# Kernel optimization log

Hardware: AMD Instinct MI355X
Metric: run time of the kernel (lower is better)

## Reference

```python
import jax, jax.numpy as jnp
import numpy as np

D_IN, D_HID, D_OUT, ITERS = 768, 256, 64, 5
LN_EPS = 1e-5


def setup_inputs() -> dict:
    key = jax.random.key(0)
    ks = jax.random.split(key, 8)
    B = 131072
    s = lambda n: 1.0 / np.sqrt(n)
    return {
        "z_mantis": jax.random.normal(ks[0], (B, D_IN), dtype=jnp.float32),
        "W1": jax.random.normal(ks[1], (D_HID, D_IN), dtype=jnp.float32) * s(D_IN),
        "b1": jnp.zeros((D_HID,), jnp.float32),
        "ln_g": jnp.ones((D_HID,), jnp.float32),
        "ln_b": jnp.zeros((D_HID,), jnp.float32),
        "W2": jax.random.normal(ks[2], (D_OUT, D_HID), dtype=jnp.float32) * s(D_HID),
        "b2": jnp.zeros((D_OUT,), jnp.float32),
        "Wr": jax.random.normal(ks[3], (D_OUT, D_IN), dtype=jnp.float32) * s(D_IN),
        "br": jnp.zeros((D_OUT,), jnp.float32),
        "Wo": jnp.linalg.qr(jax.random.normal(ks[4], (D_OUT, D_OUT), dtype=jnp.float32))[0],
        "Wv": jax.random.normal(ks[5], (D_OUT, D_OUT), dtype=jnp.float32) * s(D_OUT),
        "bv": jnp.zeros((D_OUT,), jnp.float32),
        "Wm": jax.random.normal(ks[6], (D_OUT, D_OUT), dtype=jnp.float32) * s(D_OUT),
        "bm": jnp.full((D_OUT,), 3.0, jnp.float32),
        "scale": jnp.full((1,), 2.0, jnp.float32),
    }


def _newton_schulz_whitening(X):
    # X: [B, D], returns whitened X and whitening matrix W (both [.., D])
    B, D = X.shape
    mu = jnp.mean(X, axis=0, keepdims=True)
    Xc = X - mu
    denom = jnp.float32(B - 1 if B > 1 else 1)
    sigma = (Xc.T @ Xc) / denom + 0.001 * jnp.eye(D, dtype=X.dtype)
    sigma_norm = jnp.trace(sigma) * 1.5 + 1e-6
    sigma_scaled = sigma / sigma_norm
    I = jnp.eye(D, dtype=X.dtype)
    W = I
    for _ in range(ITERS):
        P = W @ sigma_scaled @ W.T
        W = (1.5 * I - 0.5 * P) @ W
    X_white = (Xc / jnp.sqrt(sigma_norm)) @ W.T
    return X_white, W


def reference(z_mantis, W1, b1, ln_g, ln_b, W2, b2, Wr, br, Wo, Wv, bv, Wm, bm, scale):
    # pre_mlp: Linear -> LayerNorm -> GELU -> (Dropout=id in eval) -> Linear
    h = z_mantis @ W1.T + b1
    mean = jnp.mean(h, axis=-1, keepdims=True)
    var = jnp.var(h, axis=-1, keepdims=True)
    h = (h - mean) / jnp.sqrt(var + LN_EPS) * ln_g + ln_b
    h = jax.nn.gelu(h, approximate=False)
    h_latent = h @ W2.T + b2
    h_latent = h_latent + (z_mantis @ Wr.T + br)  # residual projection
    h_orth = h_latent @ Wo.T
    # B = 131072 > D_OUT, so whitening branch is always taken
    h_white, _ = _newton_schulz_whitening(h_orth)
    val = h_white @ Wv.T + bv
    mask = jax.nn.sigmoid(h_white @ Wm.T + bm)
    return val * mask * scale
```

## Files before the change

### kernel.cpp

```cpp
#include <hip/hip_runtime.h>
#include <hip/hip_bf16.h>
#include <math.h>


typedef __attribute__((ext_vector_type(8))) short short8;
typedef __attribute__((ext_vector_type(4))) float f32x4;

#define NB 131072
#define DIN 768
#define DHID 256
#define DOUT 64
#define LN_EPS 1e-5f

__device__ __forceinline__ unsigned short f2bf(float f) {
    union { float f; unsigned u; } v; v.f = f;
    return (unsigned short)((v.u + 0x7FFFu + ((v.u >> 16) & 1u)) >> 16);
}
__device__ __forceinline__ unsigned short f2bf_hu(float f) {
    return (unsigned short)((__float_as_uint(f) + 0x8000u) >> 16);
}
__device__ __forceinline__ unsigned pk2bf(float a, float b) {
    unsigned ua = __float_as_uint(a) + 0x8000u;
    unsigned ub = __float_as_uint(b) + 0x8000u;
    return __builtin_amdgcn_perm(ub, ua, 0x07060302u);
}

__global__ void k_cvt_w1(const float* __restrict__ W1, unsigned short* __restrict__ W1bf) {
    int i = blockIdx.x * 256 + threadIdx.x;
    float4 v = reinterpret_cast<const float4*>(W1)[i];
    ushort4 o;
    o.x = f2bf(v.x); o.y = f2bf(v.y); o.z = f2bf(v.z); o.w = f2bf(v.w);
    reinterpret_cast<ushort4*>(W1bf)[i] = o;
}

__global__ void k_fuse_w(const float* __restrict__ Wo, const float* __restrict__ W2,
                         const float* __restrict__ Wr, const float* __restrict__ b2,
                         const float* __restrict__ br,
                         unsigned short* __restrict__ Wabf, unsigned short* __restrict__ Wbbf,
                         float* __restrict__ c0) {
    int idx = blockIdx.x * 256 + threadIdx.x;
    if (idx < DOUT * DIN) {
        int i = idx / DIN, k = idx % DIN;
        float s = 0.f;
        #pragma unroll 8
        for (int j = 0; j < 64; j++) s += Wo[i * 64 + j] * Wr[j * DIN + k];
        Wbbf[idx] = f2bf(s);
    } else if (idx < DOUT * DIN + DOUT * DHID) {
        int e = idx - DOUT * DIN;
        int i = e / DHID, k = e % DHID;
        float s = 0.f;
        #pragma unroll 8
        for (int j = 0; j < 64; j++) s += Wo[i * 64 + j] * W2[j * DHID + k];
        Wabf[e] = f2bf(s);
    } else if (idx < DOUT * DIN + DOUT * DHID + DOUT) {
        int i = idx - (DOUT * DIN + DOUT * DHID);
        float s = 0.f;
        for (int j = 0; j < 64; j++) s += Wo[i * 64 + j] * (b2[j] + br[j]);
        c0[i] = s;
    }
}

#define ZSTR_U 20
#define ZBUF_U (64 * ZSTR_U)
#define HP_STR 264
__launch_bounds__(256, 2)
__global__ void k_main(const float* __restrict__ z,
                       const unsigned short* __restrict__ W1bf,
                       const unsigned short* __restrict__ Wbbf,
                       const unsigned short* __restrict__ Wabf,
                       const float* __restrict__ c0,
                       const float* __restrict__ b1,
                       const float* __restrict__ ln_g,
                       const float* __restrict__ ln_b,
                       float* __restrict__ X) {
    __shared__ __align__(16) unsigned smem_u[2 * ZBUF_U + (64 * HP_STR) / 2 + 256 + 256 + 64 + 64];
    unsigned* zbf = smem_u;
    unsigned short* hp = (unsigned short*)(smem_u + 2 * ZBUF_U);
    float* red1  = (float*)(smem_u + 2 * ZBUF_U + (64 * HP_STR) / 2);
    float* red2  = red1 + 256;
    float* meanb = red2 + 256;
    float* rstdb = meanb + 64;

    const int tid  = threadIdx.x;
    const int w    = tid >> 6;
    const int lane = tid & 63;
    const int q    = lane >> 4;
    const int l15  = lane & 15;
    const int m0   = blockIdx.x * 64;

    const int sr = tid >> 2;
    const int sc = (tid & 3) * 8;
    const float* zrow = z + (size_t)(m0 + sr) * DIN + sc;
    const unsigned widx = sr * ZSTR_U + (tid & 3) * 4;

    f32x4 acc1[4][4];
    f32x4 accR[4];
    #pragma unroll
    for (int mt = 0; mt < 4; mt++) {
        accR[mt] = (f32x4){0.f, 0.f, 0.f, 0.f};
        #pragma unroll
        for (int nt = 0; nt < 4; nt++) acc1[mt][nt] = (f32x4){0.f, 0.f, 0.f, 0.f};
    }

    {
        float4 f0 = *reinterpret_cast<const float4*>(zrow);
        float4 f1 = *reinterpret_cast<const float4*>(zrow + 4);
        uint4 pk = { pk2bf(f0.x, f0.y), pk2bf(f0.z, f0.w), pk2bf(f1.x, f1.y), pk2bf(f1.z, f1.w) };
        *reinterpret_cast<uint4*>(&zbf[widx]) = pk;
    }
    short8 wc[5];
    #pragma unroll
    for (int nt = 0; nt < 4; nt++)
        wc[nt] = *reinterpret_cast<const short8*>(W1bf + (size_t)(64 * w + 16 * nt + l15) * DIN + q * 8);
    wc[4] = *reinterpret_cast<const short8*>(Wbbf + (size_t)(16 * w + l15) * DIN + q * 8);
    __syncthreads();

    for (int k0 = 0; k0 < 24; k0++) {
        const int buf = k0 & 1;
        float4 g0 = {0, 0, 0, 0}, g1 = {0, 0, 0, 0};
        short8 wn[5];
        if (k0 < 23) {
            const float* zp = zrow + (k0 + 1) * 32;
            g0 = *reinterpret_cast<const float4*>(zp);
            g1 = *reinterpret_cast<const float4*>(zp + 4);
            const int kn = (k0 + 1) * 32 + q * 8;
            #pragma unroll
            for (int nt = 0; nt < 4; nt++)
                wn[nt] = *reinterpret_cast<const short8*>(W1bf + (size_t)(64 * w + 16 * nt + l15) * DIN + kn);
            wn[4] = *reinterpret_cast<const short8*>(Wbbf + (size_t)(16 * w + l15) * DIN + kn);
        }
        short8 a[4];
        #pragma unroll
        for (int mt = 0; mt < 4; mt++)
            a[mt] = *reinterpret_cast<const short8*>(&zbf[buf * ZBUF_U + (16 * mt + l15) * ZSTR_U + q * 4]);
        #pragma unroll
        for (int mt = 0; mt < 4; mt++) {
            accR[mt] = __builtin_amdgcn_mfma_f32_16x16x32_bf16(a[mt], wc[4], accR[mt], 0, 0, 0);
            #pragma unroll
            for (int nt = 0; nt < 4; nt++)
                acc1[mt][nt] = __builtin_amdgcn_mfma_f32_16x16x32_bf16(a[mt], wc[nt], acc1[mt][nt], 0, 0, 0);
        }
        if (k0 < 23) {
            uint4 pk = { pk2bf(g0.x, g0.y), pk2bf(g0.z, g0.w), pk2bf(g1.x, g1.y), pk2bf(g1.z, g1.w) };
            *reinterpret_cast<uint4*>(&zbf[(buf ^ 1) * ZBUF_U + widx]) = pk;
            #pragma unroll
            for (int i = 0; i < 5; i++) wc[i] = wn[i];
        }
        __syncthreads();
    }

    float b1v[4], gv[4], betav[4];
    #pragma unroll
    for (int nt = 0; nt < 4; nt++) {
        int col = 64 * w + 16 * nt + l15;
        b1v[nt] = b1[col]; gv[nt] = ln_g[col]; betav[nt] = ln_b[col];
    }
    #pragma unroll
    for (int mt = 0; mt < 4; mt++) {
        #pragma unroll
        for (int r = 0; r < 4; r++) {
            float s1 = 0.f, s2 = 0.f;
            #pragma unroll
            for (int nt = 0; nt < 4; nt++) {
                float x = acc1[mt][nt][r] + b1v[nt];
                s1 += x; s2 += x * x;
            }
            #pragma unroll
            for (int off = 1; off < 16; off <<= 1) {
                s1 += __shfl_xor(s1, off, 64);
                s2 += __shfl_xor(s2, off, 64);
            }
            if (l15 == 0) {
                int row = 16 * mt + 4 * q + r;
                red1[w * 64 + row] = s1; red2[w * 64 + row] = s2;
            }
        }
    }
    __syncthreads();
    if (tid < 64) {
        float s1 = red1[tid] + red1[64 + tid] + red1[128 + tid] + red1[192 + tid];
        float s2 = red2[tid] + red2[64 + tid] + red2[128 + tid] + red2[192 + tid];
        float mean = s1 * (1.f / 256.f);
        float var  = s2 * (1.f / 256.f) - mean * mean;
        meanb[tid] = mean;
        rstdb[tid] = rsqrtf(var + LN_EPS);
    }
    __syncthreads();

    #pragma unroll
    for (int mt = 0; mt < 4; mt++) {
        #pragma unroll
        for (int r = 0; r < 4; r++) {
            int row = 16 * mt + 4 * q + r;
            float mean = meanb[row], rstd = rstdb[row];
            #pragma unroll
            for (int nt = 0; nt < 4; nt++) {
                float x = acc1[mt][nt][r] + b1v[nt];
                float y = (x - mean) * rstd * gv[nt] + betav[nt];
                float g = 0.5f * y * (1.0f + erff(y * 0.70710678118654752f));
                hp[row * HP_STR + 64 * w + 16 * nt + l15] = f2bf_hu(g);
            }
        }
    }
    short8 wa_c = *reinterpret_cast<const short8*>(Wabf + (size_t)(16 * w + l15) * DHID + q * 8);
    __syncthreads();

    f32x4 acc2[4];
    #pragma unroll
    for (int mt = 0; mt < 4; mt++) acc2[mt] = accR[mt];
    for (int k = 0; k < 8; k++) {
        short8 wa_n;
        if (k < 7)
            wa_n = *reinterpret_cast<const short8*>(Wabf + (size_t)(16 * w + l15) * DHID + (k + 1) * 32 + q * 8);
        #pragma unroll
        for (int mt = 0; mt < 4; mt++) {
            short8 af = *reinterpret_cast<const short8*>(&hp[(16 * mt + l15) * HP_STR + k * 32 + q * 8]);
            acc2[mt] = __builtin_amdgcn_mfma_f32_16x16x32_bf16(af, wa_c, acc2[mt], 0, 0, 0);
        }
        if (k < 7) wa_c = wa_n;
    }
    float c0v = c0[16 * w + l15];
    #pragma unroll
    for (int mt = 0; mt < 4; mt++) {
        #pragma unroll
        for (int r = 0; r < 4; r++)
            X[(size_t)(m0 + 16 * mt + 4 * q + r) * 64 + 16 * w + l15] = acc2[mt][r] + c0v;
    }
}

__global__ void k_stats(const float* __restrict__ X, float* __restrict__ colsum,
                        float* __restrict__ XtX) {
    __shared__ float Xs[64 * 64];
    __shared__ float csb[256];
    const int t = threadIdx.x;
    const int ti = t >> 4, tj = t & 15;
    float acc[4][4] = {{0.f}};
    float cs = 0.f;
    const int base = blockIdx.x * 512;
    for (int c = 0; c < 8; c++) {
        __syncthreads();
        #pragma unroll
        for (int kk = 0; kk < 4; kk++) {
            int fi = t + 256 * kk;
            reinterpret_cast<float4*>(Xs)[fi] =
                reinterpret_cast<const float4*>(X + (size_t)(base + c * 64) * 64)[fi];
        }
        __syncthreads();
        #pragma unroll 2
        for (int r = 0; r < 64; r++) {
            float4 xa = *reinterpret_cast<const float4*>(&Xs[r * 64 + 4 * ti]);
            float4 xb = *reinterpret_cast<const float4*>(&Xs[r * 64 + 4 * tj]);
            acc[0][0] += xa.x * xb.x; acc[0][1] += xa.x * xb.y; acc[0][2] += xa.x * xb.z; acc[0][3] += xa.x * xb.w;
            acc[1][0] += xa.y * xb.x; acc[1][1] += xa.y * xb.y; acc[1][2] += xa.y * xb.z; acc[1][3] += xa.y * xb.w;
            acc[2][0] += xa.z * xb.x; acc[2][1] += xa.z * xb.y; acc[2][2] += xa.z * xb.z; acc[2][3] += xa.z * xb.w;
            acc[3][0] += xa.w * xb.x; acc[3][1] += xa.w * xb.y; acc[3][2] += xa.w * xb.z; acc[3][3] += xa.w * xb.w;
        }
        {
            int col = t & 63, r0 = (t >> 6) * 16;
            float s = 0.f;
            #pragma unroll
            for (int r = r0; r < r0 + 16; r++) s += Xs[r * 64 + col];
            cs += s;
        }
    }
    #pragma unroll
    for (int a = 0; a < 4; a++)
        #pragma unroll
        for (int b = 0; b < 4; b++)
            atomicAdd(&XtX[(4 * ti + a) * 64 + 4 * tj + b], acc[a][b]);
    csb[t] = cs;
    __syncthreads();
    if (t < 64) atomicAdd(&colsum[t], csb[t] + csb[t + 64] + csb[t + 128] + csb[t + 192]);
}

#define NSTR 68
__device__ __forceinline__ void mm64(float* __restrict__ C, const float* __restrict__ A,
                                     const float* __restrict__ B, int ti, int tj) {
    float acc[4][4] = {{0.f}};
    #pragma unroll 2
    for (int k = 0; k < 64; k += 4) {
        float4 av[4], bv[4];
        #pragma unroll
        for (int p = 0; p < 4; p++) av[p] = *reinterpret_cast<const float4*>(&A[(4 * ti + p) * NSTR + k]);
        #pragma unroll
        for (int kk = 0; kk < 4; kk++) bv[kk] = *reinterpret_cast<const float4*>(&B[(k + kk) * NSTR + 4 * tj]);
        #pragma unroll
        for (int p = 0; p < 4; p++) {
            acc[p][0] += av[p].x * bv[0].x + av[p].y * bv[1].x + av[p].z * bv[2].x + av[p].w * bv[3].x;
            acc[p][1] += av[p].x * bv[0].y + av[p].y * bv[1].y + av[p].z * bv[2].y + av[p].w * bv[3].y;
            acc[p][2] += av[p].x * bv[0].z + av[p].y * bv[1].z + av[p].z * bv[2].z + av[p].w * bv[3].z;
            acc[p][3] += av[p].x * bv[0].w + av[p].y * bv[1].w + av[p].z * bv[2].w + av[p].w * bv[3].w;
        }
    }
    #pragma unroll
    for (int p = 0; p < 4; p++)
        #pragma unroll
        for (int r = 0; r < 4; r++) C[(4 * ti + p) * NSTR + 4 * tj + r] = acc[p][r];
    __syncthreads();
}

__global__ void k_ns(const float* __restrict__ XtX, const float* __restrict__ colsum,
                     const float* __restrict__ Wv, const float* __restrict__ bv,
                     const float* __restrict__ Wm, const float* __restrict__ bm,
                     unsigned short* __restrict__ AvTbf, unsigned short* __restrict__ AmTbf,
                     float* __restrict__ cv, float* __restrict__ cm) {
    __shared__ __align__(16) float Mb[64 * NSTR], Gb[64 * NSTR], G2b[64 * NSTR],
                                   Fb[64 * NSTR], Tb[64 * NSTR];
    __shared__ float mu[64];
    __shared__ float snorm;
    const int t = threadIdx.x;
    const int ti = t >> 4, tj = t & 15;

    if (t < 64) mu[t] = colsum[t] * (1.f / (float)NB);
    __syncthreads();
    for (int idx = t; idx < 4096; idx += 256) {
        int i = idx >> 6, j = idx & 63;
        float s = (XtX[idx] - (float)NB * mu[i] * mu[j]) * (1.f / (float)(NB - 1));
        if (i == j) s += 0.001f;
        Mb[i * NSTR + j] = s;
    }
    __syncthreads();
    if (t == 0) {
        float tr = 0.f;
        for (int i = 0; i < 64; i++) tr += Mb[i * NSTR + i];
        snorm = tr * 1.5f + 1e-6f;
    }
    __syncthreads();
    const float sn = snorm;
    for (int idx = t; idx < 4096; idx += 256) {
        int i = idx >> 6, j = idx & 63;
        Mb[i * NSTR + j] /= sn;
    }
    __syncthreads();

    float *M = Mb, *G = Gb, *G2 = G2b, *F = Fb, *T = Tb;
    for (int it = 0; it < 5; it++) {
        for (int idx = t; idx < 4096; idx += 256) {
            int i = idx >> 6, j = idx & 63;
            G[i * NSTR + j] = (i == j ? 1.5f : 0.f) - 0.5f * M[i * NSTR + j];
        }
        __syncthreads();
        if (it == 0) {
            for (int idx = t; idx < 4096; idx += 256) {
                int i = idx >> 6, j = idx & 63;
                F[i * NSTR + j] = G[i * NSTR + j];
            }
            __syncthreads();
        } else {
            mm64(T, F, G, ti, tj);
            float* tmp = F; F = T; T = tmp;
        }
        if (it < 4) {
            mm64(G2, G, G, ti, tj);
            mm64(T, M, G2, ti, tj);
            float* tmp = M; M = T; T = tmp;
        }
    }
    const float rsn = rsqrtf(sn);
    float accv[4][4] = {{0.f}}, accm[4][4] = {{0.f}};
    #pragma unroll 2
    for (int k = 0; k < 64; k += 4) {
        float4 av[4];
        #pragma unroll
        for (int p = 0; p < 4; p++) av[p] = *reinterpret_cast<const float4*>(&F[(4 * ti + p) * NSTR + k]);
        #pragma unroll
        for (int r = 0; r < 4; r++) {
            float4 wv4 = *reinterpret_cast<const float4*>(&Wv[(size_t)(4 * tj + r) * 64 + k]);
            float4 wm4 = *reinterpret_cast<const float4*>(&Wm[(size_t)(4 * tj + r) * 64 + k]);
            #pragma unroll
            for (int p = 0; p < 4; p++) {
                accv[p][r] += av[p].x * wv4.x + av[p].y * wv4.y + av[p].z * wv4.z + av[p].w * wv4.w;
                accm[p][r] += av[p].x * wm4.x + av[p].y * wm4.y + av[p].z * wm4.z + av[p].w * wm4.w;
            }
        }
    }
    #pragma unroll
    for (int p = 0; p < 4; p++)
        #pragma unroll
        for (int r = 0; r < 4; r++) {
            AvTbf[(4 * tj + r) * 64 + 4 * ti + p] = f2bf_hu(rsn * accv[p][r]);
            AmTbf[(4 * tj + r) * 64 + 4 * ti + p] = f2bf_hu(rsn * accm[p][r]);
        }
    #pragma unroll
    for (int r = 0; r < 4; r++) {
        float pv = 0.f, pm = 0.f;
        #pragma unroll
        for (int p = 0; p < 4; p++) {
            pv += mu[4 * ti + p] * accv[p][r];
            pm += mu[4 * ti + p] * accm[p][r];
        }
        G2b[ti * 64 + 4 * tj + r] = pv * rsn;
        Gb[ti * 64 + 4 * tj + r]  = pm * rsn;
    }
    __syncthreads();
    if (t < 64) {
        float a = bv[t], b = bm[t];
        for (int i = 0; i < 16; i++) {
            a -= G2b[i * 64 + t];
            b -= Gb[i * 64 + t];
        }
        cv[t] = a; cm[t] = b;
    }
}

__global__ void k_out(const float* __restrict__ X,
                      const unsigned short* __restrict__ AvTbf,
                      const unsigned short* __restrict__ AmTbf,
                      const float* __restrict__ cv, const float* __restrict__ cm,
                      const float* __restrict__ scale, float* __restrict__ out) {
    const int tid  = threadIdx.x;
    const int w    = tid >> 6;
    const int lane = tid & 63;
    const int q    = lane >> 4;
    const int l15  = lane & 15;
    const int base = blockIdx.x * 64 + w * 16;

    short8 bfv[4][2], bfm[4][2];
    #pragma unroll
    for (int nt = 0; nt < 4; nt++)
        #pragma unroll
        for (int kk = 0; kk < 2; kk++) {
            bfv[nt][kk] = *reinterpret_cast<const short8*>(AvTbf + (16 * nt + l15) * 64 + kk * 32 + q * 8);
            bfm[nt][kk] = *reinterpret_cast<const short8*>(AmTbf + (16 * nt + l15) * 64 + kk * 32 + q * 8);
        }
    f32x4 av_[4], am_[4];
    #pragma unroll
    for (int nt = 0; nt < 4; nt++) {
        av_[nt] = (f32x4){0.f, 0.f, 0.f, 0.f};
        am_[nt] = (f32x4){0.f, 0.f, 0.f, 0.f};
    }
    #pragma unroll
    for (int kk = 0; kk < 2; kk++) {
        const float* xp = X + (size_t)(base + l15) * 64 + kk * 32 + q * 8;
        float4 f0 = *reinterpret_cast<const float4*>(xp);
        float4 f1 = *reinterpret_cast<const float4*>(xp + 4);
        union { unsigned u[4]; short8 s; } pk;
        pk.u[0] = pk2bf(f0.x, f0.y); pk.u[1] = pk2bf(f0.z, f0.w);
        pk.u[2] = pk2bf(f1.x, f1.y); pk.u[3] = pk2bf(f1.z, f1.w);
        #pragma unroll
        for (int nt = 0; nt < 4; nt++) {
            av_[nt] = __builtin_amdgcn_mfma_f32_16x16x32_bf16(pk.s, bfv[nt][kk], av_[nt], 0, 0, 0);
            am_[nt] = __builtin_amdgcn_mfma_f32_16x16x32_bf16(pk.s, bfm[nt][kk], am_[nt], 0, 0, 0);
        }
    }
    const float sc = scale[0];
    #pragma unroll
    for (int nt = 0; nt < 4; nt++) {
        float cvn = cv[16 * nt + l15], cmn = cm[16 * nt + l15];
        #pragma unroll
        for (int r = 0; r < 4; r++) {
            float v = av_[nt][r] + cvn;
            float m = am_[nt][r] + cmn;
            float sg = 1.f / (1.f + __expf(-m));
            out[(size_t)(base + 4 * q + r) * 64 + 16 * nt + l15] = v * sg * sc;
        }
    }
}

extern "C" void kernel_launch(void* const* d_in, const int* in_sizes, int n_in,
                              void* d_out, int out_size, void* d_ws, size_t ws_size,
                              hipStream_t stream) {
    const float* z    = (const float*)d_in[0];
    const float* W1   = (const float*)d_in[1];
    const float* b1   = (const float*)d_in[2];
    const float* ln_g = (const float*)d_in[3];
    const float* ln_b = (const float*)d_in[4];
    const float* W2   = (const float*)d_in[5];
    const float* b2   = (const float*)d_in[6];
    const float* Wr   = (const float*)d_in[7];
    const float* br   = (const float*)d_in[8];
    const float* Wo   = (const float*)d_in[9];
    const float* Wv   = (const float*)d_in[10];
    const float* bv   = (const float*)d_in[11];
    const float* Wm   = (const float*)d_in[12];
    const float* bm   = (const float*)d_in[13];
    const float* scl  = (const float*)d_in[14];

    char* ws = (char*)d_ws;
    float*          X      = (float*)(ws);
    unsigned short* W1bf   = (unsigned short*)(ws + 33554432);
    unsigned short* Wbbf   = (unsigned short*)(ws + 33947648);
    unsigned short* Wabf   = (unsigned short*)(ws + 34045952);
    float*          c0     = (float*)(ws + 34078720);
    float*          colsum = (float*)(ws + 34078976);
    float*          XtX    = (float*)(ws + 34079232);
    unsigned short* AvT    = (unsigned short*)(ws + 34095616);
    unsigned short* AmT    = (unsigned short*)(ws + 34103808);
    float*          cv     = (float*)(ws + 34112000);
    float*          cm     = (float*)(ws + 34112256);

    hipMemsetAsync((void*)colsum, 0, 256 + 16384, stream);

    k_cvt_w1<<<192, 256, 0, stream>>>(W1, W1bf);
    k_fuse_w<<<257, 256, 0, stream>>>(Wo, W2, Wr, b2, br, Wabf, Wbbf, c0);
    k_main<<<NB / 64, 256, 0, stream>>>(z, W1bf, Wbbf, Wabf, c0, b1, ln_g, ln_b, X);
    k_stats<<<256, 256, 0, stream>>>(X, colsum, XtX);
    k_ns<<<1, 256, 0, stream>>>(XtX, colsum, Wv, bv, Wm, bm, AvT, AmT, cv, cm);
    k_out<<<NB / 64, 256, 0, stream>>>(X, AvT, AmT, cv, cm, scl, (float*)d_out);
}
```

Before: 795.3 us.

## Load z fragments directly into registers, drop LDS staging and per-step barriers

The first GEMM loop no longer stages z through a double-buffered LDS tile. Each wave now loads its own z fragments straight from global memory into MFMA operand layout and converts them to bf16 in registers. This removes the LDS writes and reads and the per-iteration __syncthreads. In exchange, all four waves redundantly load the same 64x32 z slice per step, which quadruples global/L2 traffic for z, and register pressure rises from holding 16 float4 prefetch registers.

```diff
diff --git a/kernel.cpp b/kernel.cpp
--- a/kernel.cpp
+++ b/kernel.cpp
@@ -60,8 +60,6 @@
     }
 }
 
-#define ZSTR_U 20
-#define ZBUF_U (64 * ZSTR_U)
 #define HP_STR 264
 __launch_bounds__(256, 2)
 __global__ void k_main(const float* __restrict__ z,
@@ -73,13 +71,9 @@
                        const float* __restrict__ ln_g,
                        const float* __restrict__ ln_b,
                        float* __restrict__ X) {
-    __shared__ __align__(16) unsigned smem_u[2 * ZBUF_U + (64 * HP_STR) / 2 + 256 + 256 + 64 + 64];
-    unsigned* zbf = smem_u;
-    unsigned short* hp = (unsigned short*)(smem_u + 2 * ZBUF_U);
-    float* red1  = (float*)(smem_u + 2 * ZBUF_U + (64 * HP_STR) / 2);
-    float* red2  = red1 + 256;
-    float* meanb = red2 + 256;
-    float* rstdb = meanb + 64;
+    __shared__ __align__(16) unsigned short hp[64 * HP_STR];
+    __shared__ float red1[4][64], red2[4][64];
+    __shared__ float meanb[64], rstdb[64];
 
     const int tid  = threadIdx.x;
     const int w    = tid >> 6;
@@ -88,10 +82,9 @@
     const int l15  = lane & 15;
     const int m0   = blockIdx.x * 64;
 
-    const int sr = tid >> 2;
-    const int sc = (tid & 3) * 8;
-    const float* zrow = z + (size_t)(m0 + sr) * DIN + sc;
-    const unsigned widx = sr * ZSTR_U + (tid & 3) * 4;
+    const float* zr = z + (size_t)(m0 + l15) * DIN + q * 8;
+    const unsigned short* w1p = W1bf + (size_t)(64 * w + l15) * DIN + q * 8;
+    const unsigned short* wbp = Wbbf + (size_t)(16 * w + l15) * DIN + q * 8;
 
     f32x4 acc1[4][4];
     f32x4 accR[4];
@@ -102,37 +95,38 @@
         for (int nt = 0; nt < 4; nt++) acc1[mt][nt] = (f32x4){0.f, 0.f, 0.f, 0.f};
     }
 
-    {
-        float4 f0 = *reinterpret_cast<const float4*>(zrow);
-        float4 f1 = *reinterpret_cast<const float4*>(zrow + 4);
-        uint4 pk = { pk2bf(f0.x, f0.y), pk2bf(f0.z, f0.w), pk2bf(f1.x, f1.y), pk2bf(f1.z, f1.w) };
-        *reinterpret_cast<uint4*>(&zbf[widx]) = pk;
-    }
-    short8 wc[5];
-    #pragma unroll
-    for (int nt = 0; nt < 4; nt++)
-        wc[nt] = *reinterpret_cast<const short8*>(W1bf + (size_t)(64 * w + 16 * nt + l15) * DIN + q * 8);
-    wc[4] = *reinterpret_cast<const short8*>(Wbbf + (size_t)(16 * w + l15) * DIN + q * 8);
-    __syncthreads();
-
+    float4 g0[4], g1[4];
+    #pragma unroll
+    for (int mt = 0; mt < 4; mt++) {
+        const float* p = zr + mt * (16 * DIN);
+        g0[mt] = *reinterpret_cast<const float4*>(p);
+        g1[mt] = *reinterpret_cast<const float4*>(p + 4);
+    }
+
+    #pragma unroll 2
     for (int k0 = 0; k0 < 24; k0++) {
-        const int buf = k0 & 1;
-        float4 g0 = {0, 0, 0, 0}, g1 = {0, 0, 0, 0};
-        short8 wn[5];
+        float4 n0[4], n1[4];
         if (k0 < 23) {
-            const float* zp = zrow + (k0 + 1) * 32;
-            g0 = *reinterpret_cast<const float4*>(zp);
-            g1 = *reinterpret_cast<const float4*>(zp + 4);
-            const int kn = (k0 + 1) * 32 + q * 8;
-            #pragma unroll
-            for (int nt = 0; nt < 4; nt++)
-                wn[nt] = *reinterpret_cast<const short8*>(W1bf + (size_t)(64 * w + 16 * nt + l15) * DIN + kn);
-            wn[4] = *reinterpret_cast<const short8*>(Wbbf + (size_t)(16 * w + l15) * DIN + kn);
-        }
+            #pragma unroll
+            for (int mt = 0; mt < 4; mt++) {
+                const float* p = zr + mt * (16 * DIN) + (k0 + 1) * 32;
+                n0[mt] = *reinterpret_cast<const float4*>(p);
+                n1[mt] = *reinterpret_cast<const float4*>(p + 4);
+            }
+        }
+        short8 wc[5];
+        #pragma unroll
+        for (int nt = 0; nt < 4; nt++)
+            wc[nt] = *reinterpret_cast<const short8*>(w1p + (size_t)(16 * nt) * DIN + k0 * 32);
+        wc[4] = *reinterpret_cast<const short8*>(wbp + k0 * 32);
         short8 a[4];
         #pragma unroll
-        for (int mt = 0; mt < 4; mt++)
-            a[mt] = *reinterpret_cast<const short8*>(&zbf[buf * ZBUF_U + (16 * mt + l15) * ZSTR_U + q * 4]);
+        for (int mt = 0; mt < 4; mt++) {
+            union { unsigned u[4]; short8 s; } pk;
+            pk.u[0] = pk2bf(g0[mt].x, g0[mt].y); pk.u[1] = pk2bf(g0[mt].z, g0[mt].w);
+            pk.u[2] = pk2bf(g1[mt].x, g1[mt].y); pk.u[3] = pk2bf(g1[mt].z, g1[mt].w);
+            a[mt] = pk.s;
+        }
         #pragma unroll
         for (int mt = 0; mt < 4; mt++) {
             accR[mt] = __builtin_amdgcn_mfma_f32_16x16x32_bf16(a[mt], wc[4], accR[mt], 0, 0, 0);
@@ -140,13 +134,8 @@
             for (int nt = 0; nt < 4; nt++)
                 acc1[mt][nt] = __builtin_amdgcn_mfma_f32_16x16x32_bf16(a[mt], wc[nt], acc1[mt][nt], 0, 0, 0);
         }
-        if (k0 < 23) {
-            uint4 pk = { pk2bf(g0.x, g0.y), pk2bf(g0.z, g0.w), pk2bf(g1.x, g1.y), pk2bf(g1.z, g1.w) };
-            *reinterpret_cast<uint4*>(&zbf[(buf ^ 1) * ZBUF_U + widx]) = pk;
-            #pragma unroll
-            for (int i = 0; i < 5; i++) wc[i] = wn[i];
-        }
-        __syncthreads();
+        #pragma unroll
+        for (int mt = 0; mt < 4; mt++) { g0[mt] = n0[mt]; g1[mt] = n1[mt]; }
     }
 
     float b1v[4], gv[4], betav[4];
@@ -172,14 +161,14 @@
             }
             if (l15 == 0) {
                 int row = 16 * mt + 4 * q + r;
-                red1[w * 64 + row] = s1; red2[w * 64 + row] = s2;
+                red1[w][row] = s1; red2[w][row] = s2;
             }
         }
     }
     __syncthreads();
     if (tid < 64) {
-        float s1 = red1[tid] + red1[64 + tid] + red1[128 + tid] + red1[192 + tid];
-        float s2 = red2[tid] + red2[64 + tid] + red2[128 + tid] + red2[192 + tid];
+        float s1 = red1[0][tid] + red1[1][tid] + red1[2][tid] + red1[3][tid];
+        float s2 = red2[0][tid] + red2[1][tid] + red2[2][tid] + red2[3][tid];
         float mean = s1 * (1.f / 256.f);
         float var  = s2 * (1.f / 256.f) - mean * mean;
         meanb[tid] = mean;
```

Result: slower. 942.4 us (+18.5%).
